# Performance work log

Hardware: AMD Instinct MI355X
Metric: run time of the kernel (lower is better)

The kernel has to match this reference:

```python
import jax, jax.numpy as jnp
import numpy as np

GROUP_SIZE = 128
IN_FEATURES = 8192
OUT_FEATURES = 28672
TOKENS = 32


def _dequantize(qweight, qzeros, scales):
    """ExLlama q4 dequant.
    qweight: (K//8, N) int32, 8 int4 values per word packed along k.
    qzeros:  (G, N//8) int32, 8 int4 zeros per word packed along n.
    scales:  (G, N) fp16.  g = k // GROUP_SIZE; w = s * (q - (z + 1)).
    """
    shifts = jnp.arange(8, dtype=jnp.int32) * 4
    K = qweight.shape[0] * 8
    N = qweight.shape[1]
    G = qzeros.shape[0]
    # unpack weights along k: (K//8, 8, N) -> (K, N)
    q = (qweight[:, None, :] >> shifts[None, :, None]) & 15
    q = q.reshape(K, N)
    # unpack zeros along n: (G, N//8, 8) -> (G, N)
    z = (qzeros[:, :, None] >> shifts[None, None, :]) & 15
    z = z.reshape(G, N)
    # group-wise dequant: reshape k into (G, GROUP_SIZE)
    qg = q.reshape(G, GROUP_SIZE, N).astype(jnp.float16)
    zf = (z + 1).astype(jnp.float16)[:, None, :]          # ExLlama stores zero-1
    w = (qg - zf) * scales[:, None, :]                    # (G, GS, N) fp16
    return w.reshape(K, N)


def setup_inputs() -> dict:
    key = jax.random.key(0)
    k1, k2, k3, k4, k5 = jax.random.split(key, 5)
    x = jax.random.normal(k1, (TOKENS, IN_FEATURES), dtype=jnp.float16)
    qweight = jax.random.randint(k2, (IN_FEATURES // 8, OUT_FEATURES),
                                 minval=-(2**31), maxval=2**31 - 1, dtype=jnp.int32)
    qzeros = jax.random.randint(k3, (IN_FEATURES // GROUP_SIZE, OUT_FEATURES // 8),
                                minval=-(2**31), maxval=2**31 - 1, dtype=jnp.int32)
    scales = (jax.random.uniform(k4, (IN_FEATURES // GROUP_SIZE, OUT_FEATURES),
                                 dtype=jnp.float32) * 0.01 + 0.001).astype(jnp.float16)
    bias = jax.random.normal(k5, (OUT_FEATURES,), dtype=jnp.float16)
    return {"x": x, "qweight": qweight, "qzeros": qzeros,
            "scales": scales, "bias": bias}


def reference(x, qweight, qzeros, scales, bias):
    w = _dequantize(qweight, qzeros, scales)              # (K, N) fp16
    out = jnp.matmul(x.astype(jnp.float16), w)            # (T, N)
    return out + bias
```

## Files before the change

kernel.cpp:

```cpp
#include <hip/hip_runtime.h>

#define T_TOK   32
#define KDIM    8192
#define NDIM    28672
#define NGRP    64
#define NZWORDS 3584
#define NSEG    8
#define GPS     (NGRP / NSEG)

typedef _Float16 half8  __attribute__((ext_vector_type(8)));
typedef _Float16 half2v __attribute__((ext_vector_type(2)));
typedef float    f32x4  __attribute__((ext_vector_type(4)));
typedef unsigned uint4v __attribute__((ext_vector_type(4)));

__global__ __launch_bounds__(256, 3)
void exllama_gemm_atomic(const int*   __restrict__ qweight,
                         const int*   __restrict__ qzeros,
                         const float* __restrict__ scales,
                         const float* __restrict__ x,
                         const float* __restrict__ bias,
                         float*       __restrict__ out)
{
    const int lane = threadIdx.x & 63;
    const int wav  = threadIdx.x >> 6;
    const int quad = lane >> 4;
    const int l16  = lane & 15;
    const int seg  = blockIdx.y;
    const int n0   = blockIdx.x * 256 + wav * 64;

    int nc[4];
    #pragma unroll
    for (int j = 0; j < 4; ++j) nc[j] = n0 + j * 16 + l16;

    f32x4 acc[4][2];
    #pragma unroll
    for (int j = 0; j < 4; ++j)
        #pragma unroll
        for (int m = 0; m < 2; ++m)
            acc[j][m] = (f32x4){0.f, 0.f, 0.f, 0.f};

    const int g0 = seg * GPS;

    const float* xr0 = x + (size_t)l16 * KDIM + quad * 8;
    const float* xr1 = xr0 + (size_t)16 * KDIM;

    unsigned qw[2][16];
    half2v   sp[2][4], cp[2][4];

    auto load_group = [&](int g, int b) {
        #pragma unroll
        for (int j = 0; j < 4; ++j) {
            float s  = scales[(size_t)g * NDIM + nc[j]];
            int   zw = qzeros[(size_t)g * NZWORDS + (nc[j] >> 3)];
            int   z  = (zw >> ((nc[j] & 7) * 4)) & 15;
            _Float16 sh = (_Float16)s;
            _Float16 ch = (_Float16)(float)(-(1025 + z));
            sp[b][j] = (half2v){sh, sh};
            cp[b][j] = (half2v){ch, ch};
        }
        const size_t rb = (size_t)(g * 16 + quad) * NDIM;
        #pragma unroll
        for (int c = 0; c < 4; ++c)
            #pragma unroll
            for (int j = 0; j < 4; ++j)
                qw[b][c * 4 + j] = (unsigned)qweight[rb + (size_t)(c * 4) * NDIM + nc[j]];
    };

    auto compute_group = [&](int g, int b) {
        #pragma unroll
        for (int c = 0; c < 4; ++c) {
            const int kof = g * 128 + c * 32;
            f32x4 xa = *(const f32x4*)(xr0 + kof);
            f32x4 xb = *(const f32x4*)(xr0 + kof + 4);
            f32x4 xc = *(const f32x4*)(xr1 + kof);
            f32x4 xd = *(const f32x4*)(xr1 + kof + 4);
            uint4v u0, u1;
            #pragma unroll
            for (int i = 0; i < 4; ++i) {
                u0[i] = __builtin_bit_cast(unsigned, __builtin_amdgcn_cvt_pkrtz(xa[i], xb[i]));
                u1[i] = __builtin_bit_cast(unsigned, __builtin_amdgcn_cvt_pkrtz(xc[i], xd[i]));
            }
            half8 a0 = __builtin_bit_cast(half8, u0);
            half8 a1 = __builtin_bit_cast(half8, u1);
            #pragma unroll
            for (int j = 0; j < 4; ++j) {
                const unsigned w = qw[b][c * 4 + j];
                uint4v bu;
                #pragma unroll
                for (int i = 0; i < 4; ++i) {
                    unsigned t = ((w >> (4 * i)) & 0x000F000Fu) | 0x64006400u;
                    half2v th = __builtin_bit_cast(half2v, t);
                    half2v r  = (th + cp[b][j]) * sp[b][j];
                    bu[i] = __builtin_bit_cast(unsigned, r);
                }
                half8 bf = __builtin_bit_cast(half8, bu);
                acc[j][0] = __builtin_amdgcn_mfma_f32_16x16x32_f16(a0, bf, acc[j][0], 0, 0, 0);
                acc[j][1] = __builtin_amdgcn_mfma_f32_16x16x32_f16(a1, bf, acc[j][1], 0, 0, 0);
            }
        }
    };

    load_group(g0, 0);
    #pragma unroll 1
    for (int gi = 0; gi < GPS; gi += 2) {
        load_group(g0 + gi + 1, 1);
        compute_group(g0 + gi, 0);
        if (gi + 2 < GPS) load_group(g0 + gi + 2, 0);
        compute_group(g0 + gi + 1, 1);
    }

    #pragma unroll
    for (int j = 0; j < 4; ++j) {
        const int n  = n0 + j * 16 + l16;
        const float bb = bias[n] * (1.0f / NSEG);
        #pragma unroll
        for (int m = 0; m < 2; ++m)
            #pragma unroll
            for (int r = 0; r < 4; ++r) {
                const int t = m * 16 + quad * 4 + r;
                unsafeAtomicAdd(out + (size_t)t * NDIM + n, acc[j][m][r] + bb);
            }
    }
}

extern "C" void kernel_launch(void* const* d_in, const int* in_sizes, int n_in,
                              void* d_out, int out_size, void* d_ws, size_t ws_size,
                              hipStream_t stream)
{
    const float* x  = (const float*)d_in[0];
    const int* qweight = (const int*)d_in[1];
    const int* qzeros  = (const int*)d_in[2];
    const float* sc = (const float*)d_in[3];
    const float* bs = (const float*)d_in[4];
    float* out      = (float*)d_out;
    (void)d_ws; (void)ws_size;

    exllama_gemm_atomic<<<dim3(NDIM / 256, NSEG), 256, 0, stream>>>(
        qweight, qzeros, sc, x, bs, out);
}
```

Before: 239.8 us.

## Stage fp16-converted activations in LDS per K segment and double split-K

```diff
diff --git a/kernel.cpp b/kernel.cpp
--- a/kernel.cpp
+++ b/kernel.cpp
@@ -5,28 +5,53 @@
 #define NDIM    28672
 #define NGRP    64
 #define NZWORDS 3584
-#define NSEG    8
+#define NSEG    16
+#define SEGK    (KDIM / NSEG)
 #define GPS     (NGRP / NSEG)
+#define XROW    (SEGK + 8)
 
 typedef _Float16 half8  __attribute__((ext_vector_type(8)));
 typedef _Float16 half2v __attribute__((ext_vector_type(2)));
 typedef float    f32x4  __attribute__((ext_vector_type(4)));
 typedef unsigned uint4v __attribute__((ext_vector_type(4)));
 
-__global__ __launch_bounds__(256, 3)
-void exllama_gemm_atomic(const int*   __restrict__ qweight,
-                         const int*   __restrict__ qzeros,
-                         const float* __restrict__ scales,
-                         const float* __restrict__ x,
-                         const float* __restrict__ bias,
-                         float*       __restrict__ out)
+__global__ __launch_bounds__(256)
+void exllama_gemm_lds_atomic(const int*   __restrict__ qweight,
+                             const int*   __restrict__ qzeros,
+                             const float* __restrict__ scales,
+                             const float* __restrict__ x,
+                             const float* __restrict__ bias,
+                             float*       __restrict__ out)
 {
-    const int lane = threadIdx.x & 63;
-    const int wav  = threadIdx.x >> 6;
+    __shared__ alignas(16) _Float16 xs[T_TOK * XROW];
+
+    const int tid  = threadIdx.x;
+    const int lane = tid & 63;
+    const int wav  = tid >> 6;
     const int quad = lane >> 4;
     const int l16  = lane & 15;
     const int seg  = blockIdx.y;
     const int n0   = blockIdx.x * 256 + wav * 64;
+
+    {
+        const int kseg0 = seg * SEGK;
+        #pragma unroll
+        for (int it = 0; it < (T_TOK * SEGK) / (256 * 8); ++it) {
+            const int e  = it * 2048 + tid * 8;
+            const int t  = e >> 9;
+            const int kl = e & (SEGK - 1);
+            const float* xp = x + (size_t)t * KDIM + kseg0 + kl;
+            f32x4 lo = *(const f32x4*)xp;
+            f32x4 hi = *(const f32x4*)(xp + 4);
+            uint4v u;
+            #pragma unroll
+            for (int j = 0; j < 4; ++j)
+                u[j] = __builtin_bit_cast(unsigned,
+                          __builtin_amdgcn_cvt_pkrtz(lo[j], hi[j]));
+            *(uint4v*)(xs + t * XROW + kl) = u;
+        }
+    }
+    __syncthreads();
 
     int nc[4];
     #pragma unroll
@@ -40,9 +65,6 @@
             acc[j][m] = (f32x4){0.f, 0.f, 0.f, 0.f};
 
     const int g0 = seg * GPS;
-
-    const float* xr0 = x + (size_t)l16 * KDIM + quad * 8;
-    const float* xr1 = xr0 + (size_t)16 * KDIM;
 
     unsigned qw[2][16];
     half2v   sp[2][4], cp[2][4];
@@ -66,22 +88,12 @@
                 qw[b][c * 4 + j] = (unsigned)qweight[rb + (size_t)(c * 4) * NDIM + nc[j]];
     };
 
-    auto compute_group = [&](int g, int b) {
+    auto compute_group = [&](int gi, int b) {
         #pragma unroll
         for (int c = 0; c < 4; ++c) {
-            const int kof = g * 128 + c * 32;
-            f32x4 xa = *(const f32x4*)(xr0 + kof);
-            f32x4 xb = *(const f32x4*)(xr0 + kof + 4);
-            f32x4 xc = *(const f32x4*)(xr1 + kof);
-            f32x4 xd = *(const f32x4*)(xr1 + kof + 4);
-            uint4v u0, u1;
-            #pragma unroll
-            for (int i = 0; i < 4; ++i) {
-                u0[i] = __builtin_bit_cast(unsigned, __builtin_amdgcn_cvt_pkrtz(xa[i], xb[i]));
-                u1[i] = __builtin_bit_cast(unsigned, __builtin_amdgcn_cvt_pkrtz(xc[i], xd[i]));
-            }
-            half8 a0 = __builtin_bit_cast(half8, u0);
-            half8 a1 = __builtin_bit_cast(half8, u1);
+            const int kloc = gi * 128 + c * 32 + quad * 8;
+            half8 a0 = *(const half8*)(xs + l16 * XROW + kloc);
+            half8 a1 = *(const half8*)(xs + (l16 + 16) * XROW + kloc);
             #pragma unroll
             for (int j = 0; j < 4; ++j) {
                 const unsigned w = qw[b][c * 4 + j];
@@ -104,9 +116,9 @@
     #pragma unroll 1
     for (int gi = 0; gi < GPS; gi += 2) {
         load_group(g0 + gi + 1, 1);
-        compute_group(g0 + gi, 0);
+        compute_group(gi, 0);
         if (gi + 2 < GPS) load_group(g0 + gi + 2, 0);
-        compute_group(g0 + gi + 1, 1);
+        compute_group(gi + 1, 1);
     }
 
     #pragma unroll
@@ -135,6 +147,6 @@
     float* out      = (float*)d_out;
     (void)d_ws; (void)ws_size;
 
-    exllama_gemm_atomic<<<dim3(NDIM / 256, NSEG), 256, 0, stream>>>(
+    exllama_gemm_lds_atomic<<<dim3(NDIM / 256, NSEG), 256, 0, stream>>>(
         qweight, qzeros, sc, x, bs, out);
 }
```

Measured after the change: 217.4 us. 9.3% less time.
